# Kernel optimization log

Measured on AMD Instinct MI355X. Metric: run time of the kernel, lower is better.

## Reference

```python
import jax, jax.numpy as jnp
import numpy as np

B, N, D, H = 2, 2048, 1024, 16
HD = D // H

def setup_inputs() -> dict:
    key = jax.random.key(0)
    ks = jax.random.split(key, 8)
    s = lambda fan_in: 1.0 / np.sqrt(fan_in)
    return {
        "x": jax.random.normal(ks[0], (B, N, D), jnp.float32),
        "coverage": jax.random.uniform(ks[1], (B, N, 1), jnp.float32),
        "w_qkv": jax.random.normal(ks[2], (D, 3 * D), jnp.float32) * s(D),
        "w_out": jax.random.normal(ks[3], (D, D), jnp.float32) * s(D),
        "b_out": jnp.zeros((D,), jnp.float32),
        "w_ce1": jax.random.normal(ks[4], (1, D // 4), jnp.float32),
        "b_ce1": jnp.zeros((D // 4,), jnp.float32),
        "w_ce2": jax.random.normal(ks[5], (D // 4, H), jnp.float32) * s(D // 4),
        "b_ce2": jnp.zeros((H,), jnp.float32),
        "w_fg1": jax.random.normal(ks[6], (D, D // 4), jnp.float32) * s(D),
        "b_fg1": jnp.zeros((D // 4,), jnp.float32),
        "w_fg2": jax.random.normal(ks[7], (D // 4, 1), jnp.float32) * s(D // 4),
        "b_fg2": jnp.zeros((1,), jnp.float32),
    }

def reference(x, coverage, w_qkv, w_out, b_out, w_ce1, b_ce1, w_ce2, b_ce2,
              w_fg1, b_fg1, w_fg2, b_fg2):
    b, n, d = x.shape
    h = w_ce2.shape[1]
    hd = d // h
    scale = hd ** -0.5
    qkv = x @ w_qkv  # (B,N,3D)
    q, k, v = jnp.split(qkv, 3, axis=-1)
    q = q.reshape(b, n, h, hd).transpose(0, 2, 1, 3)  # (B,H,N,hd)
    k = k.reshape(b, n, h, hd).transpose(0, 2, 1, 3)
    v = v.reshape(b, n, h, hd).transpose(0, 2, 1, 3)
    attn = jnp.einsum("bhnd,bhmd->bhnm", q, k) * scale  # (B,H,N,N)
    # coverage bias: MLP(1 -> D/4 -> H), broadcast over query dim
    cov = jax.nn.silu(coverage @ w_ce1 + b_ce1) @ w_ce2 + b_ce2  # (B,N,H)
    cov_bias = cov.transpose(0, 2, 1)[:, :, None, :]  # (B,H,1,N)
    # fusion gate on mean-pooled features
    x_pooled = x.mean(axis=1)  # (B,D)
    g = jax.nn.sigmoid(jax.nn.silu(x_pooled @ w_fg1 + b_fg1) @ w_fg2 + b_fg2)  # (B,1)
    g = g[:, :, None, None]  # (B,1,1,1)
    # g*(attn+bias) + (1-g)*attn == attn + g*bias (exact same math)
    attn = attn + g * cov_bias
    attn = jax.nn.softmax(attn, axis=-1)
    out = jnp.einsum("bhnm,bhmd->bhnd", attn, v)  # (B,H,N,hd)
    out = out.transpose(0, 2, 1, 3).reshape(b, n, d)
    return out @ w_out + b_out
```

## Files before the change

### kernel.cpp

```cpp
#include <hip/hip_runtime.h>
#include <math.h>

typedef __bf16 bf16_t;
typedef __bf16 bf16x8 __attribute__((ext_vector_type(8)));
typedef __bf16 bf16x4 __attribute__((ext_vector_type(4)));
typedef float f32x4 __attribute__((ext_vector_type(4)));

#define MFMA16(a, b, c) __builtin_amdgcn_mfma_f32_16x16x32_bf16((a), (b), (c), 0, 0, 0)

constexpr int Bc = 2, Nc = 2048, Dc = 1024, Hc = 16, HDc = 64;
constexpr float C1 = 0.18033688011112042f;
constexpr float LOG2E = 1.4426950408889634f;

__device__ __forceinline__ void glds16(const bf16_t* g, bf16_t* l) {
    __builtin_amdgcn_global_load_lds(
        (const __attribute__((address_space(1))) unsigned int*)g,
        (__attribute__((address_space(3))) unsigned int*)l, 16, 0, 0);
}

__global__ __launch_bounds__(256) void f2b(const float* __restrict__ src,
                                           bf16_t* __restrict__ dst) {
    int i = (blockIdx.x * 256 + threadIdx.x) * 4;
    float4 v = *(const float4*)(src + i);
    bf16x4 o = { (bf16_t)v.x, (bf16_t)v.y, (bf16_t)v.z, (bf16_t)v.w };
    *(bf16x4*)(dst + i) = o;
}

__global__ __launch_bounds__(256) void tr64(const float* __restrict__ src,
                                            bf16_t* __restrict__ dst, int R, int C) {
    __shared__ bf16_t tile[64 * 66];
    int r0 = blockIdx.y * 64, c0 = blockIdx.x * 64;
    int t = threadIdx.x;
    int cl = t & 63, rl = t >> 6;
#pragma unroll
    for (int p = 0; p < 16; ++p) {
        int r = p * 4 + rl;
        tile[r * 66 + cl] = (bf16_t)src[(size_t)(r0 + r) * C + c0 + cl];
    }
    __syncthreads();
#pragma unroll
    for (int p = 0; p < 16; ++p) {
        int r = p * 4 + rl;
        dst[(size_t)(c0 + r) * R + r0 + cl] = tile[cl * 66 + r];
    }
}

__global__ __launch_bounds__(256) void pool_partial(const float* __restrict__ x,
                                                    float* __restrict__ pooled) {
    int blk = blockIdx.x;
    int b = blk >> 7, ch = blk & 127;
    int t = threadIdx.x;
    int c = t * 4;
    float s0 = 0.f, s1 = 0.f, s2 = 0.f, s3 = 0.f;
    for (int rr = 0; rr < 16; ++rr) {
        float4 v = *(const float4*)(x + (size_t)(b * Nc + ch * 16 + rr) * Dc + c);
        s0 += v.x; s1 += v.y; s2 += v.z; s3 += v.w;
    }
    atomicAdd(&pooled[b * Dc + c + 0], s0);
    atomicAdd(&pooled[b * Dc + c + 1], s1);
    atomicAdd(&pooled[b * Dc + c + 2], s2);
    atomicAdd(&pooled[b * Dc + c + 3], s3);
}

__global__ __launch_bounds__(256) void gate1(const float* __restrict__ pooled,
                                             const float* __restrict__ w_fg1,
                                             const float* __restrict__ b_fg1,
                                             const float* __restrict__ w_fg2,
                                             float* __restrict__ hacc) {
    int b = blockIdx.x >> 8, j = blockIdx.x & 255;
    int t = threadIdx.x;
    float p = 0.f;
#pragma unroll
    for (int i = 0; i < 4; ++i) {
        int d = t * 4 + i;
        p += pooled[b * 1024 + d] * w_fg1[d * 256 + j];
    }
#pragma unroll
    for (int off = 32; off > 0; off >>= 1) p += __shfl_down(p, off);
    __shared__ float red[4];
    if ((t & 63) == 0) red[t >> 6] = p;
    __syncthreads();
    if (t == 0) {
        float hj = (red[0] + red[1] + red[2] + red[3]) * (1.0f / 2048.0f) + b_fg1[j];
        hj = hj / (1.0f + __expf(-hj));
        atomicAdd(&hacc[b], hj * w_fg2[j]);
    }
}

__global__ __launch_bounds__(256) void covbias_k(const float* __restrict__ coverage,
                                                 const float* __restrict__ w_ce1,
                                                 const float* __restrict__ b_ce1,
                                                 const float* __restrict__ w_ce2,
                                                 const float* __restrict__ b_ce2,
                                                 const float* __restrict__ hacc,
                                                 const float* __restrict__ b_fg2,
                                                 float* __restrict__ biasbuf) {
    int t = threadIdx.x;
    int h = t & 15;
    int gn = blockIdx.x * 16 + (t >> 4);
    int b = gn >> 11, n = gn & 2047;
    float g = 1.0f / (1.0f + __expf(-(hacc[b] + b_fg2[0])));
    float c = coverage[gn];
    float acc = b_ce2[h];
    for (int j = 0; j < 256; ++j) {
        float tv = c * w_ce1[j] + b_ce1[j];
        tv = tv / (1.0f + __expf(-tv));
        acc += tv * w_ce2[j * 16 + h];
    }
    biasbuf[((size_t)b * 16 + h) * 2048 + n] = LOG2E * g * acc;
}

__global__ __launch_bounds__(256) void qkv_gemm(const bf16_t* __restrict__ Xb,
                                                const bf16_t* __restrict__ Wt,
                                                bf16_t* __restrict__ Q,
                                                bf16_t* __restrict__ Kb,
                                                bf16_t* __restrict__ Vt) {
    __shared__ __align__(16) bf16_t At[128 * 32];
    __shared__ __align__(16) bf16_t Bt[128 * 32];
    int t = threadIdx.x, w = t >> 6, lane = t & 63;
    int l16 = lane & 15, quad = lane >> 4;
    int wm = w & 1, wx = w >> 1;
    int m0 = blockIdx.x * 128;
    int n0 = blockIdx.y * 128;
    f32x4 acc[4][4] = {};
    int sw = (l16 >> 2) & 3;

    for (int k0 = 0; k0 < 1024; k0 += 32) {
#pragma unroll
        for (int i = 0; i < 2; ++i) {
            int fb = i * 4096 + w * 1024;
            int f = fb + lane * 16;
            int row = f >> 6;
            int ch = (f >> 4) & 3;
            int sc = ch ^ ((row >> 2) & 3);
            glds16(Wt + (size_t)(n0 + row) * 1024 + k0 + sc * 8, At + (fb >> 1));
            glds16(Xb + (size_t)(m0 + row) * 1024 + k0 + sc * 8, Bt + (fb >> 1));
        }
        __syncthreads();
        bf16x8 afr[4], bfr[4];
#pragma unroll
        for (int mi = 0; mi < 4; ++mi)
            afr[mi] = *(const bf16x8*)(At + (wm * 64 + mi * 16 + l16) * 32 + ((quad ^ sw) * 8));
#pragma unroll
        for (int ni = 0; ni < 4; ++ni)
            bfr[ni] = *(const bf16x8*)(Bt + (wx * 64 + ni * 16 + l16) * 32 + ((quad ^ sw) * 8));
#pragma unroll
        for (int mi = 0; mi < 4; ++mi)
#pragma unroll
            for (int ni = 0; ni < 4; ++ni)
                acc[mi][ni] = MFMA16(afr[mi], bfr[ni], acc[mi][ni]);
        __syncthreads();
    }

    int sec = n0 >> 10;
#pragma unroll
    for (int mi = 0; mi < 4; ++mi) {
        int gc = n0 + wm * 64 + mi * 16 + quad * 4;
        int dcol = gc & 1023;
        int h = dcol >> 6, hd = dcol & 63;
#pragma unroll
        for (int ni = 0; ni < 4; ++ni) {
            int gx = m0 + wx * 64 + ni * 16 + l16;
            int b = gx >> 11, n = gx & 2047;
            size_t bh = (size_t)(b * 16 + h);
            if (sec == 2) {
#pragma unroll
                for (int r = 0; r < 4; ++r)
                    Vt[(bh * 64 + hd + r) * 2048 + n] = (bf16_t)acc[mi][ni][r];
            } else {
                bf16x4 pk = { (bf16_t)acc[mi][ni][0], (bf16_t)acc[mi][ni][1],
                              (bf16_t)acc[mi][ni][2], (bf16_t)acc[mi][ni][3] };
                bf16_t* dst = (sec == 0 ? Q : Kb);
                *(bf16x4*)(dst + (bh * 2048 + n) * 64 + hd) = pk;
            }
        }
    }
}

__global__ __launch_bounds__(256) void attn_k(const bf16_t* __restrict__ Q,
                                              const bf16_t* __restrict__ Kb,
                                              const bf16_t* __restrict__ Vt,
                                              const float* __restrict__ biasbuf,
                                              bf16_t* __restrict__ O) {
    __shared__ __align__(16) bf16_t kbuf[2][64 * 64];
    __shared__ __align__(16) bf16_t vbuf[2][64 * 64];
    int t = threadIdx.x, w = t >> 6, lane = t & 63;
    int l16 = lane & 15, quad = lane >> 4;
    int bh = blockIdx.y;
    int b = bh >> 4, h = bh & 15;
    int qa = blockIdx.x * 64 + w * 16;
    const bf16_t* Qh = Q + (size_t)bh * 2048 * 64;
    const bf16_t* Kh = Kb + (size_t)bh * 2048 * 64;
    const bf16_t* Vh = Vt + (size_t)bh * 64 * 2048;
    const float* bih = biasbuf + (size_t)bh * 2048;

    int fb0 = w * 2048, fb1 = fb0 + 1024;
    int f0 = fb0 + lane * 16, f1 = fb1 + lane * 16;
    int krow0 = f0 >> 7, kch0 = ((f0 >> 4) & 7) ^ (krow0 & 7);
    int krow1 = f1 >> 7, kch1 = ((f1 >> 4) & 7) ^ (krow1 & 7);

    bf16x8 qf[2];
#pragma unroll
    for (int dh = 0; dh < 2; ++dh)
        qf[dh] = *(const bf16x8*)(Qh + (size_t)(qa + l16) * 64 + dh * 32 + quad * 8);

    f32x4 o[4] = {};
    float lsum = 0.f;
    const f32x4 zero = { 0.f, 0.f, 0.f, 0.f };
    int swl = l16 & 7;
    int qh = quad >> 1, ql = quad & 1;

    {
        glds16(Kh + (size_t)krow0 * 64 + kch0 * 8, &kbuf[0][fb0 >> 1]);
        glds16(Kh + (size_t)krow1 * 64 + kch1 * 8, &kbuf[0][fb1 >> 1]);
        glds16(Vh + (size_t)krow0 * 2048 + kch0 * 8, &vbuf[0][fb0 >> 1]);
        glds16(Vh + (size_t)krow1 * 2048 + kch1 * 8, &vbuf[0][fb1 >> 1]);
    }

    for (int it = 0; it < 32; ++it) {
        int j0 = it * 64, sel = it & 1;
        __syncthreads();
        if (it + 1 < 32) {
            int jn = j0 + 64, sn = sel ^ 1;
            glds16(Kh + (size_t)(jn + krow0) * 64 + kch0 * 8, &kbuf[sn][fb0 >> 1]);
            glds16(Kh + (size_t)(jn + krow1) * 64 + kch1 * 8, &kbuf[sn][fb1 >> 1]);
            glds16(Vh + (size_t)krow0 * 2048 + jn + kch0 * 8, &vbuf[sn][fb0 >> 1]);
            glds16(Vh + (size_t)krow1 * 2048 + jn + kch1 * 8, &vbuf[sn][fb1 >> 1]);
        }
        const bf16_t* kb = kbuf[sel];
        const bf16_t* vb = vbuf[sel];

        float4 bias[4];
#pragma unroll
        for (int kt = 0; kt < 4; ++kt)
            bias[kt] = *(const float4*)(bih + j0 + kt * 16 + quad * 4);

        f32x4 s[4];
#pragma unroll
        for (int kt = 0; kt < 4; ++kt) {
            bf16x8 kf0 = *(const bf16x8*)(kb + (kt * 16 + l16) * 64 + ((quad ^ swl) * 8));
            bf16x8 kf1 = *(const bf16x8*)(kb + (kt * 16 + l16) * 64 + (((4 + quad) ^ swl) * 8));
            s[kt] = MFMA16(kf0, qf[0], zero);
            s[kt] = MFMA16(kf1, qf[1], s[kt]);
        }

#pragma unroll
        for (int kt = 0; kt < 4; ++kt) {
            const float* bp = (const float*)&bias[kt];
#pragma unroll
            for (int r = 0; r < 4; ++r) {
                float p = __builtin_amdgcn_exp2f(s[kt][r] * C1 + bp[r]);
                s[kt][r] = p;
                lsum += p;
            }
        }

        bf16x8 pf[2];
#pragma unroll
        for (int pv = 0; pv < 2; ++pv) {
            bf16x8 tmp;
#pragma unroll
            for (int i = 0; i < 4; ++i) {
                tmp[i]     = (bf16_t)s[2 * pv][i];
                tmp[i + 4] = (bf16_t)s[2 * pv + 1][i];
            }
            pf[pv] = tmp;
        }

#pragma unroll
        for (int dt = 0; dt < 4; ++dt) {
            const bf16_t* vrow = vb + (dt * 16 + l16) * 64 + ql * 4;
#pragma unroll
            for (int pv = 0; pv < 2; ++pv) {
                int c0 = (pv * 4 + qh) ^ swl;
                int c1 = (pv * 4 + 2 + qh) ^ swl;
                bf16x4 va = *(const bf16x4*)(vrow + c0 * 8);
                bf16x4 vc = *(const bf16x4*)(vrow + c1 * 8);
                bf16x8 vf = __builtin_shufflevector(va, vc, 0, 1, 2, 3, 4, 5, 6, 7);
                o[dt] = MFMA16(pf[pv], vf, o[dt]);
            }
        }
    }

    lsum += __shfl_xor(lsum, 16);
    lsum += __shfl_xor(lsum, 32);
    float rinv[4];
#pragma unroll
    for (int r = 0; r < 4; ++r)
        rinv[r] = 1.0f / __shfl(lsum, quad * 4 + r);
#pragma unroll
    for (int dt = 0; dt < 4; ++dt)
#pragma unroll
        for (int r = 0; r < 4; ++r) {
            int row = qa + quad * 4 + r;
            O[(size_t)(b * 2048 + row) * 1024 + h * 64 + dt * 16 + l16] =
                (bf16_t)(o[dt][r] * rinv[r]);
        }
}

__global__ __launch_bounds__(256) void out_gemm(const bf16_t* __restrict__ A,
                                                const bf16_t* __restrict__ Wt,
                                                const float* __restrict__ bias,
                                                float* __restrict__ Cout) {
    __shared__ __align__(16) bf16_t At[128 * 32];
    __shared__ __align__(16) bf16_t Bt[128 * 32];
    int t = threadIdx.x, w = t >> 6, lane = t & 63;
    int l16 = lane & 15, quad = lane >> 4;
    int wm = w & 1, wx = w >> 1;
    int m0 = blockIdx.x * 128;
    int n0 = blockIdx.y * 128;
    f32x4 acc[4][4] = {};
    int sw = (l16 >> 2) & 3;

    for (int k0 = 0; k0 < 1024; k0 += 32) {
#pragma unroll
        for (int i = 0; i < 2; ++i) {
            int fb = i * 4096 + w * 1024;
            int f = fb + lane * 16;
            int row = f >> 6;
            int ch = (f >> 4) & 3;
            int sc = ch ^ ((row >> 2) & 3);
            glds16(Wt + (size_t)(n0 + row) * 1024 + k0 + sc * 8, At + (fb >> 1));
            glds16(A + (size_t)(m0 + row) * 1024 + k0 + sc * 8, Bt + (fb >> 1));
        }
        __syncthreads();
        bf16x8 afr[4], bfr[4];
#pragma unroll
        for (int mi = 0; mi < 4; ++mi)
            afr[mi] = *(const bf16x8*)(At + (wm * 64 + mi * 16 + l16) * 32 + ((quad ^ sw) * 8));
#pragma unroll
        for (int ni = 0; ni < 4; ++ni)
            bfr[ni] = *(const bf16x8*)(Bt + (wx * 64 + ni * 16 + l16) * 32 + ((quad ^ sw) * 8));
#pragma unroll
        for (int mi = 0; mi < 4; ++mi)
#pragma unroll
            for (int ni = 0; ni < 4; ++ni)
                acc[mi][ni] = MFMA16(afr[mi], bfr[ni], acc[mi][ni]);
        __syncthreads();
    }

#pragma unroll
    for (int mi = 0; mi < 4; ++mi) {
        int gc = n0 + wm * 64 + mi * 16 + quad * 4;
        float4 bv = *(const float4*)(bias + gc);
#pragma unroll
        for (int ni = 0; ni < 4; ++ni) {
            int gx = m0 + wx * 64 + ni * 16 + l16;
            float4 ov = { acc[mi][ni][0] + bv.x, acc[mi][ni][1] + bv.y,
                          acc[mi][ni][2] + bv.z, acc[mi][ni][3] + bv.w };
            *(float4*)(Cout + (size_t)gx * 1024 + gc) = ov;
        }
    }
}

extern "C" void kernel_launch(void* const* d_in, const int* in_sizes, int n_in,
                              void* d_out, int out_size, void* d_ws, size_t ws_size,
                              hipStream_t stream) {
    const float* x     = (const float*)d_in[0];
    const float* cov   = (const float*)d_in[1];
    const float* w_qkv = (const float*)d_in[2];
    const float* w_out = (const float*)d_in[3];
    const float* b_out = (const float*)d_in[4];
    const float* w_ce1 = (const float*)d_in[5];
    const float* b_ce1 = (const float*)d_in[6];
    const float* w_ce2 = (const float*)d_in[7];
    const float* b_ce2 = (const float*)d_in[8];
    const float* w_fg1 = (const float*)d_in[9];
    const float* b_fg1 = (const float*)d_in[10];
    const float* w_fg2 = (const float*)d_in[11];
    const float* b_fg2 = (const float*)d_in[12];

    char* ws = (char*)d_ws;
    bf16_t* Wt     = (bf16_t*)(ws);
    bf16_t* WoT    = (bf16_t*)(ws + 6291456);
    bf16_t* Xb     = (bf16_t*)(ws + 8388608);
    bf16_t* Qb     = (bf16_t*)(ws + 16777216);
    bf16_t* Kbb    = (bf16_t*)(ws + 25165824);
    bf16_t* Vt     = (bf16_t*)(ws + 33554432);
    bf16_t* Ob     = (bf16_t*)(ws + 41943040);
    float*  pooled = (float*)(ws + 50331648);
    float*  hacc   = (float*)(ws + 50339840);
    float*  biasb  = (float*)(ws + 50340096);

    hipMemsetAsync(pooled, 0, 2 * 1024 * sizeof(float), stream);
    hipMemsetAsync(hacc, 0, 2 * sizeof(float), stream);
    f2b<<<4096, 256, 0, stream>>>(x, Xb);
    tr64<<<dim3(48, 16), 256, 0, stream>>>(w_qkv, Wt, 1024, 3072);
    tr64<<<dim3(16, 16), 256, 0, stream>>>(w_out, WoT, 1024, 1024);
    pool_partial<<<256, 256, 0, stream>>>(x, pooled);
    gate1<<<512, 256, 0, stream>>>(pooled, w_fg1, b_fg1, w_fg2, hacc);
    covbias_k<<<256, 256, 0, stream>>>(cov, w_ce1, b_ce1, w_ce2, b_ce2, hacc, b_fg2, biasb);
    qkv_gemm<<<dim3(32, 24), 256, 0, stream>>>(Xb, Wt, Qb, Kbb, Vt);
    attn_k<<<dim3(32, 32), 256, 0, stream>>>(Qb, Kbb, Vt, biasb, Ob);
    out_gemm<<<dim3(32, 8), 256, 0, stream>>>(Ob, WoT, b_out, (float*)d_out);
}
```

Measured before the change: 271.5 us.

## Fuse prep kernels, widen attention query tiles, permute V layout, shrink out GEMM tiles

Merges the x-to-bf16 conversion with the mean-pool reduction and the two weight transposes into single launches, and folds the two memsets into one. The attention kernel now processes 32 query rows per wave, reusing each loaded K/V fragment across two query groups. It computes row sums with MFMA against a ones vector instead of a shuffle reduction, and reads V with one 16-byte load because V is stored in a permuted column order. The output GEMM uses 64-wide N tiles to double the block count. Together these cut launches and LDS traffic, at the cost of more registers per thread in attention and halved grid size there.

```diff
diff --git a/kernel.cpp b/kernel.cpp
--- a/kernel.cpp
+++ b/kernel.cpp
@@ -18,18 +18,37 @@
         (__attribute__((address_space(3))) unsigned int*)l, 16, 0, 0);
 }
 
-__global__ __launch_bounds__(256) void f2b(const float* __restrict__ src,
-                                           bf16_t* __restrict__ dst) {
-    int i = (blockIdx.x * 256 + threadIdx.x) * 4;
-    float4 v = *(const float4*)(src + i);
-    bf16x4 o = { (bf16_t)v.x, (bf16_t)v.y, (bf16_t)v.z, (bf16_t)v.w };
-    *(bf16x4*)(dst + i) = o;
-}
-
-__global__ __launch_bounds__(256) void tr64(const float* __restrict__ src,
-                                            bf16_t* __restrict__ dst, int R, int C) {
+__global__ __launch_bounds__(256) void prep_x(const float* __restrict__ x,
+                                              bf16_t* __restrict__ Xb,
+                                              float* __restrict__ pooled) {
+    int row0 = blockIdx.x * 8;
+    int b = row0 >> 11;
+    int c = threadIdx.x * 4;
+    float s0 = 0.f, s1 = 0.f, s2 = 0.f, s3 = 0.f;
+#pragma unroll
+    for (int rr = 0; rr < 8; ++rr) {
+        size_t off = (size_t)(row0 + rr) * 1024 + c;
+        float4 v = *(const float4*)(x + off);
+        bf16x4 o = { (bf16_t)v.x, (bf16_t)v.y, (bf16_t)v.z, (bf16_t)v.w };
+        *(bf16x4*)(Xb + off) = o;
+        s0 += v.x; s1 += v.y; s2 += v.z; s3 += v.w;
+    }
+    atomicAdd(&pooled[b * 1024 + c + 0], s0);
+    atomicAdd(&pooled[b * 1024 + c + 1], s1);
+    atomicAdd(&pooled[b * 1024 + c + 2], s2);
+    atomicAdd(&pooled[b * 1024 + c + 3], s3);
+}
+
+__global__ __launch_bounds__(256) void tr64f(const float* __restrict__ w_qkv,
+                                             const float* __restrict__ w_out,
+                                             bf16_t* __restrict__ Wt,
+                                             bf16_t* __restrict__ WoT) {
     __shared__ bf16_t tile[64 * 66];
-    int r0 = blockIdx.y * 64, c0 = blockIdx.x * 64;
+    const float* src; bf16_t* dst; int C, cx;
+    if (blockIdx.x < 48) { src = w_qkv; dst = Wt; C = 3072; cx = blockIdx.x; }
+    else                 { src = w_out; dst = WoT; C = 1024; cx = blockIdx.x - 48; }
+    const int R = 1024;
+    int r0 = blockIdx.y * 64, c0 = cx * 64;
     int t = threadIdx.x;
     int cl = t & 63, rl = t >> 6;
 #pragma unroll
@@ -43,23 +62,6 @@
         int r = p * 4 + rl;
         dst[(size_t)(c0 + r) * R + r0 + cl] = tile[cl * 66 + r];
     }
-}
-
-__global__ __launch_bounds__(256) void pool_partial(const float* __restrict__ x,
-                                                    float* __restrict__ pooled) {
-    int blk = blockIdx.x;
-    int b = blk >> 7, ch = blk & 127;
-    int t = threadIdx.x;
-    int c = t * 4;
-    float s0 = 0.f, s1 = 0.f, s2 = 0.f, s3 = 0.f;
-    for (int rr = 0; rr < 16; ++rr) {
-        float4 v = *(const float4*)(x + (size_t)(b * Nc + ch * 16 + rr) * Dc + c);
-        s0 += v.x; s1 += v.y; s2 += v.z; s3 += v.w;
-    }
-    atomicAdd(&pooled[b * Dc + c + 0], s0);
-    atomicAdd(&pooled[b * Dc + c + 1], s1);
-    atomicAdd(&pooled[b * Dc + c + 2], s2);
-    atomicAdd(&pooled[b * Dc + c + 3], s3);
 }
 
 __global__ __launch_bounds__(256) void gate1(const float* __restrict__ pooled,
@@ -164,9 +166,10 @@
             int b = gx >> 11, n = gx & 2047;
             size_t bh = (size_t)(b * 16 + h);
             if (sec == 2) {
+                int np = (n & ~31) + ((n >> 2) & 3) * 8 + ((n >> 4) & 1) * 4 + (n & 3);
 #pragma unroll
                 for (int r = 0; r < 4; ++r)
-                    Vt[(bh * 64 + hd + r) * 2048 + n] = (bf16_t)acc[mi][ni][r];
+                    Vt[(bh * 64 + hd + r) * 2048 + np] = (bf16_t)acc[mi][ni][r];
             } else {
                 bf16x4 pk = { (bf16_t)acc[mi][ni][0], (bf16_t)acc[mi][ni][1],
                               (bf16_t)acc[mi][ni][2], (bf16_t)acc[mi][ni][3] };
@@ -188,7 +191,7 @@
     int l16 = lane & 15, quad = lane >> 4;
     int bh = blockIdx.y;
     int b = bh >> 4, h = bh & 15;
-    int qa = blockIdx.x * 64 + w * 16;
+    int qa = blockIdx.x * 128 + w * 32;
     const bf16_t* Qh = Q + (size_t)bh * 2048 * 64;
     const bf16_t* Kh = Kb + (size_t)bh * 2048 * 64;
     const bf16_t* Vh = Vt + (size_t)bh * 64 * 2048;
@@ -199,16 +202,20 @@
     int krow0 = f0 >> 7, kch0 = ((f0 >> 4) & 7) ^ (krow0 & 7);
     int krow1 = f1 >> 7, kch1 = ((f1 >> 4) & 7) ^ (krow1 & 7);
 
-    bf16x8 qf[2];
-#pragma unroll
-    for (int dh = 0; dh < 2; ++dh)
-        qf[dh] = *(const bf16x8*)(Qh + (size_t)(qa + l16) * 64 + dh * 32 + quad * 8);
-
-    f32x4 o[4] = {};
-    float lsum = 0.f;
+    bf16x8 qf[2][2];
+#pragma unroll
+    for (int g = 0; g < 2; ++g)
+#pragma unroll
+        for (int dh = 0; dh < 2; ++dh)
+            qf[g][dh] = *(const bf16x8*)(Qh + (size_t)(qa + g * 16 + l16) * 64 + dh * 32 + quad * 8);
+
+    f32x4 o[2][4] = {};
+    f32x4 osum[2] = {};
     const f32x4 zero = { 0.f, 0.f, 0.f, 0.f };
     int swl = l16 & 7;
-    int qh = quad >> 1, ql = quad & 1;
+    bf16x8 ones;
+#pragma unroll
+    for (int i = 0; i < 8; ++i) ones[i] = (bf16_t)1.0f;
 
     {
         glds16(Kh + (size_t)krow0 * 64 + kch0 * 8, &kbuf[0][fb0 >> 1]);
@@ -235,104 +242,118 @@
         for (int kt = 0; kt < 4; ++kt)
             bias[kt] = *(const float4*)(bih + j0 + kt * 16 + quad * 4);
 
-        f32x4 s[4];
+        f32x4 s[4][2];
 #pragma unroll
         for (int kt = 0; kt < 4; ++kt) {
             bf16x8 kf0 = *(const bf16x8*)(kb + (kt * 16 + l16) * 64 + ((quad ^ swl) * 8));
             bf16x8 kf1 = *(const bf16x8*)(kb + (kt * 16 + l16) * 64 + (((4 + quad) ^ swl) * 8));
-            s[kt] = MFMA16(kf0, qf[0], zero);
-            s[kt] = MFMA16(kf1, qf[1], s[kt]);
+#pragma unroll
+            for (int g = 0; g < 2; ++g) {
+                s[kt][g] = MFMA16(kf0, qf[g][0], zero);
+                s[kt][g] = MFMA16(kf1, qf[g][1], s[kt][g]);
+            }
         }
 
 #pragma unroll
         for (int kt = 0; kt < 4; ++kt) {
             const float* bp = (const float*)&bias[kt];
 #pragma unroll
+            for (int g = 0; g < 2; ++g)
+#pragma unroll
+                for (int r = 0; r < 4; ++r)
+                    s[kt][g][r] = __builtin_amdgcn_exp2f(s[kt][g][r] * C1 + bp[r]);
+        }
+
+        bf16x8 pf[2][2];
+#pragma unroll
+        for (int g = 0; g < 2; ++g)
+#pragma unroll
+            for (int pv = 0; pv < 2; ++pv) {
+                bf16x8 tmp;
+#pragma unroll
+                for (int i = 0; i < 4; ++i) {
+                    tmp[i]     = (bf16_t)s[2 * pv][g][i];
+                    tmp[i + 4] = (bf16_t)s[2 * pv + 1][g][i];
+                }
+                pf[g][pv] = tmp;
+            }
+
+#pragma unroll
+        for (int dt = 0; dt < 4; ++dt) {
+            const bf16_t* vrow = vb + (dt * 16 + l16) * 64;
+#pragma unroll
+            for (int pv = 0; pv < 2; ++pv) {
+                bf16x8 vf = *(const bf16x8*)(vrow + (((pv * 4 + quad) ^ swl) * 8));
+#pragma unroll
+                for (int g = 0; g < 2; ++g)
+                    o[g][dt] = MFMA16(pf[g][pv], vf, o[g][dt]);
+            }
+        }
+#pragma unroll
+        for (int g = 0; g < 2; ++g) {
+            osum[g] = MFMA16(pf[g][0], ones, osum[g]);
+            osum[g] = MFMA16(pf[g][1], ones, osum[g]);
+        }
+    }
+
+#pragma unroll
+    for (int g = 0; g < 2; ++g) {
+        float rinv[4];
+#pragma unroll
+        for (int r = 0; r < 4; ++r) rinv[r] = 1.0f / osum[g][r];
+#pragma unroll
+        for (int dt = 0; dt < 4; ++dt)
+#pragma unroll
             for (int r = 0; r < 4; ++r) {
-                float p = __builtin_amdgcn_exp2f(s[kt][r] * C1 + bp[r]);
-                s[kt][r] = p;
-                lsum += p;
+                int row = qa + g * 16 + quad * 4 + r;
+                O[(size_t)(b * 2048 + row) * 1024 + h * 64 + dt * 16 + l16] =
+                    (bf16_t)(o[g][dt][r] * rinv[r]);
             }
-        }
-
-        bf16x8 pf[2];
-#pragma unroll
-        for (int pv = 0; pv < 2; ++pv) {
-            bf16x8 tmp;
-#pragma unroll
-            for (int i = 0; i < 4; ++i) {
-                tmp[i]     = (bf16_t)s[2 * pv][i];
-                tmp[i + 4] = (bf16_t)s[2 * pv + 1][i];
-            }
-            pf[pv] = tmp;
-        }
-
-#pragma unroll
-        for (int dt = 0; dt < 4; ++dt) {
-            const bf16_t* vrow = vb + (dt * 16 + l16) * 64 + ql * 4;
-#pragma unroll
-            for (int pv = 0; pv < 2; ++pv) {
-                int c0 = (pv * 4 + qh) ^ swl;
-                int c1 = (pv * 4 + 2 + qh) ^ swl;
-                bf16x4 va = *(const bf16x4*)(vrow + c0 * 8);
-                bf16x4 vc = *(const bf16x4*)(vrow + c1 * 8);
-                bf16x8 vf = __builtin_shufflevector(va, vc, 0, 1, 2, 3, 4, 5, 6, 7);
-                o[dt] = MFMA16(pf[pv], vf, o[dt]);
-            }
-        }
-    }
-
-    lsum += __shfl_xor(lsum, 16);
-    lsum += __shfl_xor(lsum, 32);
-    float rinv[4];
-#pragma unroll
-    for (int r = 0; r < 4; ++r)
-        rinv[r] = 1.0f / __shfl(lsum, quad * 4 + r);
-#pragma unroll
-    for (int dt = 0; dt < 4; ++dt)
-#pragma unroll
-        for (int r = 0; r < 4; ++r) {
-            int row = qa + quad * 4 + r;
-            O[(size_t)(b * 2048 + row) * 1024 + h * 64 + dt * 16 + l16] =
-                (bf16_t)(o[dt][r] * rinv[r]);
-        }
+    }
 }
 
 __global__ __launch_bounds__(256) void out_gemm(const bf16_t* __restrict__ A,
                                                 const bf16_t* __restrict__ Wt,
                                                 const float* __restrict__ bias,
                                                 float* __restrict__ Cout) {
-    __shared__ __align__(16) bf16_t At[128 * 32];
+    __shared__ __align__(16) bf16_t At[64 * 32];
     __shared__ __align__(16) bf16_t Bt[128 * 32];
     int t = threadIdx.x, w = t >> 6, lane = t & 63;
     int l16 = lane & 15, quad = lane >> 4;
     int wm = w & 1, wx = w >> 1;
     int m0 = blockIdx.x * 128;
-    int n0 = blockIdx.y * 128;
-    f32x4 acc[4][4] = {};
+    int n0 = blockIdx.y * 64;
+    f32x4 acc[2][4] = {};
     int sw = (l16 >> 2) & 3;
 
     for (int k0 = 0; k0 < 1024; k0 += 32) {
-#pragma unroll
-        for (int i = 0; i < 2; ++i) {
-            int fb = i * 4096 + w * 1024;
+        {
+            int fb = w * 1024;
             int f = fb + lane * 16;
             int row = f >> 6;
             int ch = (f >> 4) & 3;
             int sc = ch ^ ((row >> 2) & 3);
             glds16(Wt + (size_t)(n0 + row) * 1024 + k0 + sc * 8, At + (fb >> 1));
+        }
+#pragma unroll
+        for (int i = 0; i < 2; ++i) {
+            int fb = w * 2048 + i * 1024;
+            int f = fb + lane * 16;
+            int row = f >> 6;
+            int ch = (f >> 4) & 3;
+            int sc = ch ^ ((row >> 2) & 3);
             glds16(A + (size_t)(m0 + row) * 1024 + k0 + sc * 8, Bt + (fb >> 1));
         }
         __syncthreads();
-        bf16x8 afr[4], bfr[4];
-#pragma unroll
-        for (int mi = 0; mi < 4; ++mi)
-            afr[mi] = *(const bf16x8*)(At + (wm * 64 + mi * 16 + l16) * 32 + ((quad ^ sw) * 8));
+        bf16x8 afr[2], bfr[4];
+#pragma unroll
+        for (int mi = 0; mi < 2; ++mi)
+            afr[mi] = *(const bf16x8*)(At + (wm * 32 + mi * 16 + l16) * 32 + ((quad ^ sw) * 8));
 #pragma unroll
         for (int ni = 0; ni < 4; ++ni)
             bfr[ni] = *(const bf16x8*)(Bt + (wx * 64 + ni * 16 + l16) * 32 + ((quad ^ sw) * 8));
 #pragma unroll
-        for (int mi = 0; mi < 4; ++mi)
+        for (int mi = 0; mi < 2; ++mi)
 #pragma unroll
             for (int ni = 0; ni < 4; ++ni)
                 acc[mi][ni] = MFMA16(afr[mi], bfr[ni], acc[mi][ni]);
@@ -340,8 +361,8 @@
     }
 
 #pragma unroll
-    for (int mi = 0; mi < 4; ++mi) {
-        int gc = n0 + wm * 64 + mi * 16 + quad * 4;
+    for (int mi = 0; mi < 2; ++mi) {
+        int gc = n0 + wm * 32 + mi * 16 + quad * 4;
         float4 bv = *(const float4*)(bias + gc);
 #pragma unroll
         for (int ni = 0; ni < 4; ++ni) {
@@ -382,15 +403,12 @@
     float*  hacc   = (float*)(ws + 50339840);
     float*  biasb  = (float*)(ws + 50340096);
 
-    hipMemsetAsync(pooled, 0, 2 * 1024 * sizeof(float), stream);
-    hipMemsetAsync(hacc, 0, 2 * sizeof(float), stream);
-    f2b<<<4096, 256, 0, stream>>>(x, Xb);
-    tr64<<<dim3(48, 16), 256, 0, stream>>>(w_qkv, Wt, 1024, 3072);
-    tr64<<<dim3(16, 16), 256, 0, stream>>>(w_out, WoT, 1024, 1024);
-    pool_partial<<<256, 256, 0, stream>>>(x, pooled);
+    hipMemsetAsync(pooled, 0, 8192 + 256, stream);
+    prep_x<<<512, 256, 0, stream>>>(x, Xb, pooled);
+    tr64f<<<dim3(64, 16), 256, 0, stream>>>(w_qkv, w_out, Wt, WoT);
     gate1<<<512, 256, 0, stream>>>(pooled, w_fg1, b_fg1, w_fg2, hacc);
     covbias_k<<<256, 256, 0, stream>>>(cov, w_ce1, b_ce1, w_ce2, b_ce2, hacc, b_fg2, biasb);
     qkv_gemm<<<dim3(32, 24), 256, 0, stream>>>(Xb, Wt, Qb, Kbb, Vt);
-    attn_k<<<dim3(32, 32), 256, 0, stream>>>(Qb, Kbb, Vt, biasb, Ob);
-    out_gemm<<<dim3(32, 8), 256, 0, stream>>>(Ob, WoT, b_out, (float*)d_out);
-}
+    attn_k<<<dim3(16, 32), 256, 0, stream>>>(Qb, Kbb, Vt, biasb, Ob);
+    out_gemm<<<dim3(32, 16), 256, 0, stream>>>(Ob, WoT, b_out, (float*)d_out);
+}
```

Result: no change. 272.1 us (+0.2%).
